# Kernel tuning notes

Measured on AMD Instinct MI355X. Metric: run time of the kernel, lower is better.

## Reference

```python
import jax, jax.numpy as jnp
import numpy as np

B, S, H, D = 4, 2048, 16, 128

def setup_inputs() -> dict:
    key = jax.random.key(0)
    kq, kk, kv = jax.random.split(key, 3)
    shape = (B, S, H, D)
    return {
        "q": jax.random.normal(kq, shape, dtype=jnp.float32),
        "k": jax.random.normal(kk, shape, dtype=jnp.float32),
        "v": jax.random.normal(kv, shape, dtype=jnp.float32),
    }

def reference(q, k, v):
    # Fused recurrent linear attention (causal, unnormalized):
    #   H_t = H_{t-1} + k_t v_t^T ;  o_t = (scale * q_t) @ H_t
    scale = jnp.asarray(q.shape[-1], q.dtype) ** -0.5
    # move seq axis to front for scan: [S, B, H, D]
    qs = jnp.moveaxis(q, 1, 0) * scale
    ks = jnp.moveaxis(k, 1, 0)
    vs = jnp.moveaxis(v, 1, 0)

    def step(h, qkv):
        qt, kt, vt = qkv  # each [B, H, D]
        h = h + kt[..., :, None] * vt[..., None, :]  # [B, H, Dk, Dv]
        o = jnp.einsum('bhk,bhkv->bhv', qt, h)       # [B, H, Dv]
        return h, o

    h0 = jnp.zeros((q.shape[0], q.shape[2], q.shape[3], v.shape[3]), dtype=q.dtype)
    _, o = jax.lax.scan(step, h0, (qs, ks, vs))
    return jnp.moveaxis(o, 0, 1)  # [B, S, H, D]
```

## Files before the change

kernel.cpp:

```cpp
#include <hip/hip_runtime.h>


#define Bc 4
#define Sq 2048
#define Hh 16
#define Dd 128
#define RS (Hh * Dd)
#define Cc 128
#define NCH (Sq / Cc)
#define BHt (Bc * Hh)
#define SCALE 0.08838834764831845f

using frag_ab = __attribute__((ext_vector_type(8))) short;
using frag_cd = __attribute__((ext_vector_type(4))) float;

__device__ __forceinline__ unsigned short f2bf(float f) {
  union { float f; unsigned u; } x; x.f = f;
  unsigned r = x.u + 0x7FFFu + ((x.u >> 16) & 1u);
  return (unsigned short)(r >> 16);
}
__device__ __forceinline__ int sw64(int r, int c) {
  return r * 64 + ((((c >> 3) ^ (r & 7)) << 3) | (c & 7));
}
__device__ __forceinline__ int sw128(int r, int c) {
  return r * 128 + ((((c >> 3) ^ (r & 15)) << 3) | (c & 7));
}
__device__ __forceinline__ int swKT(int dk, int t) {
  return dk * 128 + ((((t >> 3) ^ (dk ^ (dk >> 4))) & 15) << 3) + (t & 7);
}
__device__ __forceinline__ int swVT(int dv, int t) {
  return dv * 128 + ((((t >> 3) ^ dv) & 15) << 3) + (t & 7);
}

__global__ __launch_bounds__(256) void phA_state(const float* __restrict__ kg,
                                                 const float* __restrict__ vg,
                                                 unsigned short* __restrict__ st) {
  __shared__ unsigned short KT[128 * 128];
  __shared__ unsigned short VT[16 * 128];
  const int tid = threadIdx.x;
  const int bh = blockIdx.x & 63, slice = blockIdx.x >> 6;
  const int b = bh >> 4, h = bh & 15;
  const int dv0 = slice * 16;
  const size_t base = (size_t)b * Sq * RS + (size_t)h * Dd;
  const int w = tid >> 6, L = tid & 63, li = L & 15, q4 = L >> 4;
  const int kdk0 = (tid & 31) * 4;
  const int ktg4 = (tid >> 5) * 4;
  const int vdv0l = (tid & 3) * 4;
  const int vt0 = (tid >> 2) * 2;

  float4 rk[4][4];
  float4 rv[2];
  auto prefetch = [&](int n) {
    const size_t t0g = (size_t)n * Cc;
#pragma unroll
    for (int p = 0; p < 4; ++p) {
      const int t0 = p * 32 + ktg4;
#pragma unroll
      for (int i = 0; i < 4; ++i)
        rk[p][i] = *(const float4*)(kg + base + (t0g + t0 + i) * (size_t)RS + kdk0);
    }
#pragma unroll
    for (int i = 0; i < 2; ++i)
      rv[i] = *(const float4*)(vg + base + (t0g + vt0 + i) * (size_t)RS + dv0 + vdv0l);
  };

  frag_cd acc[2];
  acc[0] = (frag_cd){0.f, 0.f, 0.f, 0.f};
  acc[1] = (frag_cd){0.f, 0.f, 0.f, 0.f};
  prefetch(0);
  const size_t sbb = (size_t)bh * NCH * (128 * 128);

  for (int n = 0; n < NCH; ++n) {
    __syncthreads();
#pragma unroll
    for (int p = 0; p < 4; ++p) {
      const int t0 = p * 32 + ktg4;
#pragma unroll
      for (int j = 0; j < 4; ++j) {
        ushort4 u;
        u.x = f2bf(((const float*)&rk[p][0])[j]);
        u.y = f2bf(((const float*)&rk[p][1])[j]);
        u.z = f2bf(((const float*)&rk[p][2])[j]);
        u.w = f2bf(((const float*)&rk[p][3])[j]);
        *(ushort4*)&KT[swKT(kdk0 + j, t0)] = u;
      }
    }
#pragma unroll
    for (int j = 0; j < 4; ++j) {
      ushort2 u;
      u.x = f2bf(((const float*)&rv[0])[j]);
      u.y = f2bf(((const float*)&rv[1])[j]);
      *(ushort2*)&VT[swVT(vdv0l + j, vt0)] = u;
    }
    if (n + 1 < NCH) prefetch(n + 1);
    __syncthreads();
    const size_t sb = sbb + (size_t)n * (128 * 128);
#pragma unroll
    for (int nt = 0; nt < 2; ++nt)
#pragma unroll
      for (int r = 0; r < 4; ++r) {
        const int dv = dv0 + 4 * q4 + r;
        const int dk = 32 * w + 16 * nt + li;
        st[sb + (size_t)dv * 128 + dk] = f2bf(acc[nt][r]);
      }
#pragma unroll
    for (int kt = 0; kt < 4; ++kt) {
      frag_ab af = *(const frag_ab*)&VT[swVT(li, 32 * kt + 8 * q4)];
#pragma unroll
      for (int nt = 0; nt < 2; ++nt) {
        frag_ab bf = *(const frag_ab*)&KT[swKT(32 * w + 16 * nt + li, 32 * kt + 8 * q4)];
        acc[nt] = __builtin_amdgcn_mfma_f32_16x16x32_bf16(af, bf, acc[nt], 0, 0, 0);
      }
    }
  }
}

__global__ __launch_bounds__(256) void phB_out(const float* __restrict__ qg,
                                               const float* __restrict__ kg,
                                               const float* __restrict__ vg,
                                               const unsigned short* __restrict__ st,
                                               float* __restrict__ o) {
  __shared__ unsigned short QP[128 * 128];
  __shared__ unsigned short Bb[128 * 64];
  const int tid = threadIdx.x;
  const int bid = blockIdx.x;
  const int bh = bid >> 4, n = bid & 15;
  const int b = bh >> 4, h = bh & 15;
  const size_t cbase = (size_t)b * Sq * RS + (size_t)n * Cc * RS + (size_t)h * Dd;
  const size_t sb = (size_t)(bh * 16 + n) * (128 * 128);
  const int w = tid >> 6, L = tid & 63;
  const int wr = w >> 1, wc = w & 1, li = L & 15, q4 = L >> 4;

#pragma unroll
  for (int it = 0; it < 16; ++it) {
    const int f = it * 256 + tid;
    const int t = f >> 5;
    const int c0 = (f & 31) << 2;
    const float4 q4v = *(const float4*)(qg + cbase + (size_t)t * RS + c0);
    ushort4 qu;
    qu.x = f2bf(q4v.x * SCALE); qu.y = f2bf(q4v.y * SCALE);
    qu.z = f2bf(q4v.z * SCALE); qu.w = f2bf(q4v.w * SCALE);
    *(ushort4*)&QP[sw128(t, c0)] = qu;
  }
  frag_cd accO[4][4], accP[4][4];
#pragma unroll
  for (int i = 0; i < 4; ++i)
#pragma unroll
    for (int j = 0; j < 4; ++j) {
      accO[i][j] = (frag_cd){0.f, 0.f, 0.f, 0.f};
      accP[i][j] = (frag_cd){0.f, 0.f, 0.f, 0.f};
    }

  for (int half = 0; half < 2; ++half) {
    __syncthreads();
#pragma unroll
    for (int it = 0; it < 4; ++it) {
      const int f = it * 256 + tid;
      const int dv = f >> 3;
      const int c8 = (f & 7) << 3;
      const uint4 hv = *(const uint4*)(st + sb + (size_t)dv * 128 + 64 * half + c8);
      *(uint4*)&Bb[sw64(dv, c8)] = hv;
    }
    __syncthreads();
#pragma unroll
    for (int kt = 0; kt < 2; ++kt) {
      const int ktg = 2 * half + kt;
      frag_ab af[4], bf_[4];
#pragma unroll
      for (int mt = 0; mt < 4; ++mt)
        af[mt] = *(const frag_ab*)&QP[sw128(64 * wr + 16 * mt + li, 32 * ktg + 8 * q4)];
#pragma unroll
      for (int nt = 0; nt < 4; ++nt)
        bf_[nt] = *(const frag_ab*)&Bb[sw64(64 * wc + 16 * nt + li, 32 * kt + 8 * q4)];
#pragma unroll
      for (int mt = 0; mt < 4; ++mt)
#pragma unroll
        for (int nt = 0; nt < 4; ++nt)
          accO[mt][nt] = __builtin_amdgcn_mfma_f32_16x16x32_bf16(af[mt], bf_[nt], accO[mt][nt], 0, 0, 0);
    }
  }

  for (int half = 0; half < 2; ++half) {
    __syncthreads();
#pragma unroll
    for (int it = 0; it < 8; ++it) {
      const int f = it * 256 + tid;
      const int t = f >> 4;
      const int c0 = (f & 15) << 2;
      const float4 k4v = *(const float4*)(kg + cbase + (size_t)t * RS + 64 * half + c0);
      ushort4 ku;
      ku.x = f2bf(k4v.x); ku.y = f2bf(k4v.y); ku.z = f2bf(k4v.z); ku.w = f2bf(k4v.w);
      *(ushort4*)&Bb[sw64(t, c0)] = ku;
    }
    __syncthreads();
    if (64 * wc <= 64 * wr + 63) {
#pragma unroll
      for (int kt = 0; kt < 2; ++kt) {
        const int ktg = 2 * half + kt;
        frag_ab af[4], bf_[4];
#pragma unroll
        for (int mt = 0; mt < 4; ++mt)
          af[mt] = *(const frag_ab*)&QP[sw128(64 * wr + 16 * mt + li, 32 * ktg + 8 * q4)];
#pragma unroll
        for (int nt = 0; nt < 4; ++nt)
          bf_[nt] = *(const frag_ab*)&Bb[sw64(64 * wc + 16 * nt + li, 32 * kt + 8 * q4)];
#pragma unroll
        for (int mt = 0; mt < 4; ++mt)
#pragma unroll
          for (int nt = 0; nt < 4; ++nt)
            if (64 * wc + 16 * nt <= 64 * wr + 16 * mt + 15)
              accP[mt][nt] = __builtin_amdgcn_mfma_f32_16x16x32_bf16(af[mt], bf_[nt], accP[mt][nt], 0, 0, 0);
      }
    }
  }
  __syncthreads();
#pragma unroll
  for (int mt = 0; mt < 4; ++mt)
#pragma unroll
    for (int nt = 0; nt < 4; ++nt) {
      const int t0 = 64 * wr + 16 * mt + 4 * q4;
      const int s = 64 * wc + 16 * nt + li;
#pragma unroll
      for (int r = 0; r < 4; ++r) {
        const int t = t0 + r;
        QP[sw128(t, s)] = (s <= t) ? f2bf(accP[mt][nt][r]) : (unsigned short)0;
      }
    }

  for (int half = 0; half < 2; ++half) {
    __syncthreads();
#pragma unroll
    for (int it = 0; it < 8; ++it) {
      const int sl = (tid & 15) | ((it & 3) << 4);
      const int c0 = ((tid >> 4) | ((it >> 2) << 4)) << 2;
      const int s = 64 * half + sl;
      const float4 v4v = *(const float4*)(vg + cbase + (size_t)s * RS + c0);
      Bb[sw64(c0 + 0, sl)] = f2bf(v4v.x);
      Bb[sw64(c0 + 1, sl)] = f2bf(v4v.y);
      Bb[sw64(c0 + 2, sl)] = f2bf(v4v.z);
      Bb[sw64(c0 + 3, sl)] = f2bf(v4v.w);
    }
    __syncthreads();
#pragma unroll
    for (int kt = 0; kt < 2; ++kt) {
      const int ktg = 2 * half + kt;
      if (32 * ktg > 64 * wr + 63) continue;
      frag_ab af[4], bf_[4];
#pragma unroll
      for (int mt = 0; mt < 4; ++mt)
        af[mt] = *(const frag_ab*)&QP[sw128(64 * wr + 16 * mt + li, 32 * ktg + 8 * q4)];
#pragma unroll
      for (int nt = 0; nt < 4; ++nt)
        bf_[nt] = *(const frag_ab*)&Bb[sw64(64 * wc + 16 * nt + li, 32 * kt + 8 * q4)];
#pragma unroll
      for (int mt = 0; mt < 4; ++mt)
#pragma unroll
        for (int nt = 0; nt < 4; ++nt)
          if (32 * ktg <= 64 * wr + 16 * mt + 15)
            accO[mt][nt] = __builtin_amdgcn_mfma_f32_16x16x32_bf16(af[mt], bf_[nt], accO[mt][nt], 0, 0, 0);
    }
  }
#pragma unroll
  for (int mt = 0; mt < 4; ++mt)
#pragma unroll
    for (int nt = 0; nt < 4; ++nt)
#pragma unroll
      for (int r = 0; r < 4; ++r) {
        const int t = 64 * wr + 16 * mt + 4 * q4 + r;
        const int dv = 64 * wc + 16 * nt + li;
        o[cbase + (size_t)t * RS + dv] = accO[mt][nt][r];
      }
}

extern "C" void kernel_launch(void* const* d_in, const int* in_sizes, int n_in,
                              void* d_out, int out_size, void* d_ws, size_t ws_size,
                              hipStream_t stream) {
  const float* q = (const float*)d_in[0];
  const float* k = (const float*)d_in[1];
  const float* v = (const float*)d_in[2];
  float* o = (float*)d_out;
  unsigned short* st = (unsigned short*)d_ws;
  hipLaunchKernelGGL(phA_state, dim3(BHt * 8), dim3(256), 0, stream, k, v, st);
  hipLaunchKernelGGL(phB_out, dim3(BHt * NCH), dim3(256), 0, stream, q, k, v, st, o);
}
```

Before: 276.4 us.

## Split state-accumulation scan into segments and combine segment prefixes in output kernel

The phase-A state kernel now splits the 16 chunks into 4 independent segments, each computing local prefix states, which gives 4x more blocks than the serial scan over the whole sequence. Each segment writes local partial states plus its total, and the output kernel rebuilds the full prefix state by summing up to four bf16 state matrices before its Q·H matmul. The output kernel's block index mapping is also reordered to interleave heads across chunks. The trade-off is extra state reads and bf16 summation in phase B, with some added rounding error from combining bf16 partials.

Measured after the change: 289.4 us. +4.7%, slower.

```diff
diff --git a/kernel.cpp b/kernel.cpp
--- a/kernel.cpp
+++ b/kernel.cpp
@@ -9,6 +9,8 @@
 #define Cc 128
 #define NCH (Sq / Cc)
 #define BHt (Bc * Hh)
+#define NSEG 4
+#define CPS (NCH / NSEG)
 #define SCALE 0.08838834764831845f
 
 using frag_ab = __attribute__((ext_vector_type(8))) short;
@@ -18,6 +20,10 @@
   union { float f; unsigned u; } x; x.f = f;
   unsigned r = x.u + 0x7FFFu + ((x.u >> 16) & 1u);
   return (unsigned short)(r >> 16);
+}
+__device__ __forceinline__ float bf2f(unsigned short u) {
+  union { unsigned u; float f; } x; x.u = ((unsigned)u) << 16;
+  return x.f;
 }
 __device__ __forceinline__ int sw64(int r, int c) {
   return r * 64 + ((((c >> 3) ^ (r & 7)) << 3) | (c & 7));
@@ -38,7 +44,9 @@
   __shared__ unsigned short KT[128 * 128];
   __shared__ unsigned short VT[16 * 128];
   const int tid = threadIdx.x;
-  const int bh = blockIdx.x & 63, slice = blockIdx.x >> 6;
+  const int bh = blockIdx.x & 63;
+  const int slice = (blockIdx.x >> 6) & 7;
+  const int seg = blockIdx.x >> 9;
   const int b = bh >> 4, h = bh & 15;
   const int dv0 = slice * 16;
   const size_t base = (size_t)b * Sq * RS + (size_t)h * Dd;
@@ -67,34 +75,12 @@
   frag_cd acc[2];
   acc[0] = (frag_cd){0.f, 0.f, 0.f, 0.f};
   acc[1] = (frag_cd){0.f, 0.f, 0.f, 0.f};
-  prefetch(0);
+  const int n0 = seg * CPS;
+  prefetch(n0);
   const size_t sbb = (size_t)bh * NCH * (128 * 128);
 
-  for (int n = 0; n < NCH; ++n) {
-    __syncthreads();
-#pragma unroll
-    for (int p = 0; p < 4; ++p) {
-      const int t0 = p * 32 + ktg4;
-#pragma unroll
-      for (int j = 0; j < 4; ++j) {
-        ushort4 u;
-        u.x = f2bf(((const float*)&rk[p][0])[j]);
-        u.y = f2bf(((const float*)&rk[p][1])[j]);
-        u.z = f2bf(((const float*)&rk[p][2])[j]);
-        u.w = f2bf(((const float*)&rk[p][3])[j]);
-        *(ushort4*)&KT[swKT(kdk0 + j, t0)] = u;
-      }
-    }
-#pragma unroll
-    for (int j = 0; j < 4; ++j) {
-      ushort2 u;
-      u.x = f2bf(((const float*)&rv[0])[j]);
-      u.y = f2bf(((const float*)&rv[1])[j]);
-      *(ushort2*)&VT[swVT(vdv0l + j, vt0)] = u;
-    }
-    if (n + 1 < NCH) prefetch(n + 1);
-    __syncthreads();
-    const size_t sb = sbb + (size_t)n * (128 * 128);
+  auto store_acc = [&](int slot) {
+    const size_t sb = sbb + (size_t)slot * (128 * 128);
 #pragma unroll
     for (int nt = 0; nt < 2; ++nt)
 #pragma unroll
@@ -103,6 +89,33 @@
         const int dk = 32 * w + 16 * nt + li;
         st[sb + (size_t)dv * 128 + dk] = f2bf(acc[nt][r]);
       }
+  };
+
+  for (int j = 0; j < CPS; ++j) {
+    __syncthreads();
+#pragma unroll
+    for (int p = 0; p < 4; ++p) {
+      const int t0 = p * 32 + ktg4;
+#pragma unroll
+      for (int jj = 0; jj < 4; ++jj) {
+        ushort4 u;
+        u.x = f2bf(((const float*)&rk[p][0])[jj]);
+        u.y = f2bf(((const float*)&rk[p][1])[jj]);
+        u.z = f2bf(((const float*)&rk[p][2])[jj]);
+        u.w = f2bf(((const float*)&rk[p][3])[jj]);
+        *(ushort4*)&KT[swKT(kdk0 + jj, t0)] = u;
+      }
+    }
+#pragma unroll
+    for (int jj = 0; jj < 4; ++jj) {
+      ushort2 u;
+      u.x = f2bf(((const float*)&rv[0])[jj]);
+      u.y = f2bf(((const float*)&rv[1])[jj]);
+      *(ushort2*)&VT[swVT(vdv0l + jj, vt0)] = u;
+    }
+    if (j + 1 < CPS) prefetch(n0 + j + 1);
+    __syncthreads();
+    if (j > 0) store_acc(n0 + j);
 #pragma unroll
     for (int kt = 0; kt < 4; ++kt) {
       frag_ab af = *(const frag_ab*)&VT[swVT(li, 32 * kt + 8 * q4)];
@@ -113,6 +126,7 @@
       }
     }
   }
+  if (seg + 1 < NSEG) store_acc(n0);
 }
 
 __global__ __launch_bounds__(256) void phB_out(const float* __restrict__ qg,
@@ -124,10 +138,12 @@
   __shared__ unsigned short Bb[128 * 64];
   const int tid = threadIdx.x;
   const int bid = blockIdx.x;
-  const int bh = bid >> 4, n = bid & 15;
+  const int bh = bid & 63, n = bid >> 6;
   const int b = bh >> 4, h = bh & 15;
   const size_t cbase = (size_t)b * Sq * RS + (size_t)n * Cc * RS + (size_t)h * Dd;
-  const size_t sb = (size_t)(bh * 16 + n) * (128 * 128);
+  const size_t sbh = (size_t)bh * NCH * (128 * 128);
+  const int sseg = n >> 2, jj = n & 3;
+  const int nmat = sseg + (jj ? 1 : 0);
   const int w = tid >> 6, L = tid & 63;
   const int wr = w >> 1, wc = w & 1, li = L & 15, q4 = L >> 4;
 
@@ -151,32 +167,65 @@
       accP[i][j] = (frag_cd){0.f, 0.f, 0.f, 0.f};
     }
 
-  for (int half = 0; half < 2; ++half) {
-    __syncthreads();
-#pragma unroll
-    for (int it = 0; it < 4; ++it) {
-      const int f = it * 256 + tid;
-      const int dv = f >> 3;
-      const int c8 = (f & 7) << 3;
-      const uint4 hv = *(const uint4*)(st + sb + (size_t)dv * 128 + 64 * half + c8);
-      *(uint4*)&Bb[sw64(dv, c8)] = hv;
-    }
-    __syncthreads();
-#pragma unroll
-    for (int kt = 0; kt < 2; ++kt) {
-      const int ktg = 2 * half + kt;
-      frag_ab af[4], bf_[4];
-#pragma unroll
-      for (int mt = 0; mt < 4; ++mt)
-        af[mt] = *(const frag_ab*)&QP[sw128(64 * wr + 16 * mt + li, 32 * ktg + 8 * q4)];
-#pragma unroll
-      for (int nt = 0; nt < 4; ++nt)
-        bf_[nt] = *(const frag_ab*)&Bb[sw64(64 * wc + 16 * nt + li, 32 * kt + 8 * q4)];
-#pragma unroll
-      for (int mt = 0; mt < 4; ++mt)
+  if (nmat > 0) {
+    for (int half = 0; half < 2; ++half) {
+      __syncthreads();
+      if (nmat == 1) {
+        const int slot = sseg ? 0 : n;
+#pragma unroll
+        for (int it = 0; it < 4; ++it) {
+          const int f = it * 256 + tid;
+          const int dv = f >> 3;
+          const int c8 = (f & 7) << 3;
+          const uint4 hv = *(const uint4*)(st + sbh + ((size_t)slot << 14) +
+                                           (size_t)dv * 128 + 64 * half + c8);
+          *(uint4*)&Bb[sw64(dv, c8)] = hv;
+        }
+      } else {
+#pragma unroll
+        for (int it = 0; it < 4; ++it) {
+          const int f = it * 256 + tid;
+          const int dv = f >> 3;
+          const int c8 = (f & 7) << 3;
+          float s8[8];
+#pragma unroll
+          for (int e = 0; e < 8; ++e) s8[e] = 0.f;
+          for (int m = 0; m < nmat; ++m) {
+            const int slot = (m < sseg) ? (m << 2) : n;
+            const uint4 hv = *(const uint4*)(st + sbh + ((size_t)slot << 14) +
+                                             (size_t)dv * 128 + 64 * half + c8);
+            const unsigned hw[4] = {hv.x, hv.y, hv.z, hv.w};
+#pragma unroll
+            for (int e = 0; e < 4; ++e) {
+              s8[2 * e + 0] += bf2f((unsigned short)(hw[e] & 0xFFFFu));
+              s8[2 * e + 1] += bf2f((unsigned short)(hw[e] >> 16));
+            }
+          }
+          unsigned pk[4];
+#pragma unroll
+          for (int e = 0; e < 4; ++e)
+            pk[e] = (unsigned)f2bf(s8[2 * e]) | ((unsigned)f2bf(s8[2 * e + 1]) << 16);
+          uint4 hv; hv.x = pk[0]; hv.y = pk[1]; hv.z = pk[2]; hv.w = pk[3];
+          *(uint4*)&Bb[sw64(dv, c8)] = hv;
+        }
+      }
+      __syncthreads();
+#pragma unroll
+      for (int kt = 0; kt < 2; ++kt) {
+        const int ktg = 2 * half + kt;
+        frag_ab af[4], bf_[4];
+#pragma unroll
+        for (int mt = 0; mt < 4; ++mt)
+          af[mt] = *(const frag_ab*)&QP[sw128(64 * wr + 16 * mt + li, 32 * ktg + 8 * q4)];
 #pragma unroll
         for (int nt = 0; nt < 4; ++nt)
-          accO[mt][nt] = __builtin_amdgcn_mfma_f32_16x16x32_bf16(af[mt], bf_[nt], accO[mt][nt], 0, 0, 0);
+          bf_[nt] = *(const frag_ab*)&Bb[sw64(64 * wc + 16 * nt + li, 32 * kt + 8 * q4)];
+#pragma unroll
+        for (int mt = 0; mt < 4; ++mt)
+#pragma unroll
+          for (int nt = 0; nt < 4; ++nt)
+            accO[mt][nt] = __builtin_amdgcn_mfma_f32_16x16x32_bf16(af[mt], bf_[nt], accO[mt][nt], 0, 0, 0);
+      }
     }
   }
 
@@ -280,6 +329,6 @@
   const float* v = (const float*)d_in[2];
   float* o = (float*)d_out;
   unsigned short* st = (unsigned short*)d_ws;
-  hipLaunchKernelGGL(phA_state, dim3(BHt * 8), dim3(256), 0, stream, k, v, st);
+  hipLaunchKernelGGL(phA_state, dim3(BHt * 8 * NSEG), dim3(256), 0, stream, k, v, st);
   hipLaunchKernelGGL(phB_out, dim3(BHt * NCH), dim3(256), 0, stream, q, k, v, st, o);
 }
```
